# Performance work log

Hardware: AMD Instinct MI355X
Metric: run time of the kernel (lower is better)

## Reference

```python
import jax, jax.numpy as jnp
import numpy as np

HIDDEN = 128
HEADS = 8
HEAD_DIM = HIDDEN // HEADS  # 16
N_NODE_TYPES = 3
N_EDGE_TYPES = 5
N_SRC = 50000
N_DST = 50000
N_EDGES = 800000
SCALE = float(np.sqrt(HEAD_DIM))


def setup_inputs() -> dict:
    key = jax.random.key(0)
    ks = jax.random.split(key, 12)
    lim = 1.0 / np.sqrt(HIDDEN)  # torch Linear default init range
    # xavier_uniform for [H, d, d] relation tensors: gain*sqrt(6/(fan_in+fan_out))
    xav = float(np.sqrt(6.0 / (HEAD_DIM + HEAD_DIM)))
    return {
        "x_src": jax.random.normal(ks[0], (N_SRC, HIDDEN), jnp.float32),
        "x_dst": jax.random.normal(ks[1], (N_DST, HIDDEN), jnp.float32),
        "edge_index": jax.random.randint(ks[2], (2, N_EDGES), 0, N_DST),
        "src_type": 0,
        "edge_type": 1,
        "dst_type": 2,
        "k_w": jax.random.uniform(ks[3], (N_NODE_TYPES, HIDDEN, HIDDEN), jnp.float32, -lim, lim),
        "k_b": jax.random.uniform(ks[4], (N_NODE_TYPES, HIDDEN), jnp.float32, -lim, lim),
        "q_w": jax.random.uniform(ks[5], (N_NODE_TYPES, HIDDEN, HIDDEN), jnp.float32, -lim, lim),
        "q_b": jax.random.uniform(ks[6], (N_NODE_TYPES, HIDDEN), jnp.float32, -lim, lim),
        "v_w": jax.random.uniform(ks[7], (N_NODE_TYPES, HIDDEN, HIDDEN), jnp.float32, -lim, lim),
        "v_b": jax.random.uniform(ks[8], (N_NODE_TYPES, HIDDEN), jnp.float32, -lim, lim),
        "relation_att": jax.random.uniform(ks[9], (N_EDGE_TYPES, HEADS, HEAD_DIM, HEAD_DIM), jnp.float32, -xav, xav),
        "relation_msg": jax.random.uniform(ks[10], (N_EDGE_TYPES, HEADS, HEAD_DIM, HEAD_DIM), jnp.float32, -xav, xav),
        "relation_pri": jnp.ones((N_EDGE_TYPES, HEADS), jnp.float32),
    }


def reference(x_src, x_dst, edge_index, src_type, edge_type, dst_type,
              k_w, k_b, q_w, q_b, v_w, v_b,
              relation_att, relation_msg, relation_pri):
    n_dst = x_dst.shape[0]
    # relation-specific node projections (torch Linear: x @ W.T + b)
    k = (x_src @ k_w[src_type].T + k_b[src_type]).reshape(-1, HEADS, HEAD_DIM)
    v = (x_src @ v_w[src_type].T + v_b[src_type]).reshape(-1, HEADS, HEAD_DIM)
    q = (x_dst @ q_w[dst_type].T + q_b[dst_type]).reshape(-1, HEADS, HEAD_DIM)

    src_idx, dst_idx = edge_index[0], edge_index[1]
    # gather + per-edge relation matmul: [E, H, d]
    k_edge = jnp.einsum('ehi,hio->eho', k[src_idx], relation_att[edge_type])
    att = (k_edge * q[dst_idx]).sum(-1) / SCALE + relation_pri[edge_type][None, :]  # [E, H]

    # segmented softmax over incoming edges per dst node.
    # torch scatter_reduce amax starts from a zero-initialized buffer -> max(0, seg_max)
    seg_max = jnp.maximum(jax.ops.segment_max(att, dst_idx, num_segments=n_dst), 0.0)
    att_exp = jnp.exp(att - seg_max[dst_idx])
    seg_sum = jnp.maximum(jax.ops.segment_sum(att_exp, dst_idx, num_segments=n_dst), 1e-8)
    att_n = att_exp / seg_sum[dst_idx]  # [E, H]

    # messages + weighted scatter-add aggregation
    msg = jnp.einsum('ehi,hio->eho', v[src_idx], relation_msg[edge_type])  # [E, H, d]
    out = jax.ops.segment_sum(att_n[..., None] * msg, dst_idx, num_segments=n_dst)
    return out.reshape(n_dst, HIDDEN)
```

## Files before the change

### kernel.cpp

```cpp
#include <hip/hip_runtime.h>

#define HIDDEN 128
#define HEADS 8
#define HDIM 16
#define BW 64

typedef unsigned int uint;
typedef unsigned short ushort;
typedef __attribute__((ext_vector_type(8))) short bfrag;
typedef __attribute__((ext_vector_type(4))) float f32x4;

__device__ inline ushort f2bf(float f) {
    uint u = __float_as_uint(f);
    uint r = ((u >> 16) & 1u) + 0x7fffu;
    return (ushort)((u + r) >> 16);
}
__device__ inline float bf2f(ushort h) { return __uint_as_float((uint)h << 16); }
__device__ inline float bfl(uint u) { return __uint_as_float(u << 16); }
__device__ inline float bfh(uint u) { return __uint_as_float(u & 0xffff0000u); }

__device__ inline int frag_addr(int k, int n) {
    int ks = k >> 5, kr = k & 31, nt = n >> 4;
    int lane = ((kr >> 3) << 4) | (n & 15);
    return ((ks * 8 + nt) * 64 + lane) * 8 + (kr & 7);
}

__global__ void k1a_weights_zero(
    const float* __restrict__ k_w, const float* __restrict__ k_b,
    const float* __restrict__ q_w, const float* __restrict__ q_b,
    const float* __restrict__ v_w, const float* __restrict__ v_b,
    const float* __restrict__ r_att, const float* __restrict__ r_msg,
    const int* __restrict__ stp, const int* __restrict__ etp, const int* __restrict__ dtp,
    ushort* __restrict__ WkHi, ushort* __restrict__ WvHi, ushort* __restrict__ WqHi,
    float* __restrict__ bk, float* __restrict__ bv, float* __restrict__ bq,
    int* __restrict__ deg, int n_dst)
{
    int idx = blockIdx.x * 256 + threadIdx.x;
    for (int i = idx; i < n_dst; i += 64 * 256) deg[i] = 0;

    int st = stp[0], et = etp[0], dt = dtp[0];
    int c = idx >> 7, j = idx & 127;
    int h = j >> 4, o = j & 15;
    const float* kw = k_w + (size_t)st * HIDDEN * HIDDEN;
    const float* vw = v_w + (size_t)st * HIDDEN * HIDDEN;
    const float* ra = r_att + (size_t)et * HEADS * HDIM * HDIM + h * HDIM * HDIM + o;
    const float* rm = r_msg + (size_t)et * HEADS * HDIM * HDIM + h * HDIM * HDIM + o;
    float sk = 0.f, sv = 0.f;
#pragma unroll
    for (int i = 0; i < HDIM; ++i) {
        sk += kw[(h * HDIM + i) * HIDDEN + c] * ra[i * HDIM];
        sv += vw[(h * HDIM + i) * HIDDEN + c] * rm[i * HDIM];
    }
    float sq = q_w[(size_t)dt * HIDDEN * HIDDEN + (size_t)j * HIDDEN + c];
    int fa = frag_addr(c, j);
    WkHi[fa] = f2bf(sk);
    WvHi[fa] = f2bf(sv);
    WqHi[fa] = f2bf(sq);
    if (idx < HIDDEN) {
        float sb = 0.f, sbv = 0.f;
#pragma unroll
        for (int i = 0; i < HDIM; ++i) {
            sb  += k_b[st * HIDDEN + h * HDIM + i] * ra[i * HDIM];
            sbv += v_b[st * HIDDEN + h * HDIM + i] * rm[i * HDIM];
        }
        bk[idx] = sb;
        bv[idx] = sbv;
        bq[idx] = q_b[dt * HIDDEN + idx];
    }
}

__global__ __launch_bounds__(256, 5) void k1b_proj_countfill(
    const float* __restrict__ x_src, const float* __restrict__ x_dst,
    const ushort* __restrict__ WkHi, const ushort* __restrict__ WvHi,
    const ushort* __restrict__ WqHi,
    const float* __restrict__ bk, const float* __restrict__ bv,
    const float* __restrict__ bq,
    ushort* __restrict__ kr16, ushort* __restrict__ vm16,
    float* __restrict__ qout, int n_src, int n_dst, int nsb, int nprojb,
    const int* __restrict__ ei, int* __restrict__ deg,
    ushort* __restrict__ bucket, int n_edges, int nfb)
{
    __shared__ float xs[32 * 132];
    int blk = blockIdx.x;

    if (blk & 1) {
        int fidx = blk >> 1;
        if (fidx >= nfb) return;
        int e = fidx * 256 + threadIdx.x;
        if (e >= n_edges) return;
        int s = ei[e];
        int d = ei[n_edges + e];
        int r = atomicAdd(&deg[d], 1);
        if (r < BW) bucket[(size_t)d * BW + r] = (ushort)s;
        return;
    }

    int pidx = blk >> 1;
    if (pidx >= nprojb) return;
    int is_src = (pidx < nsb) ? 1 : 0;
    int brow0 = (is_src ? pidx : pidx - nsb) * 32;
    int n = is_src ? n_src : n_dst;
    const float* x = is_src ? x_src : x_dst;
    int t = threadIdx.x;

    {
        const float4* xg = (const float4*)x;
#pragma unroll
        for (int k = 0; k < 4; ++k) {
            int fi = t + k * 256;
            int r = fi >> 5, c4 = fi & 31;
            int row = brow0 + r;
            float4 v = xg[(size_t)(row < n ? row : n - 1) * 32 + c4];
            *(float4*)&xs[r * 132 + c4 * 4] = v;
        }
    }
    __syncthreads();

    int w = t >> 6, l = t & 63;
    int l15 = l & 15, kgrp = l >> 4;
    int nthalf = w & 1;
    int rtile = w >> 1;
    int rowbase = brow0 + rtile * 16;

    bfrag ahi[4];
#pragma unroll
    for (int ks = 0; ks < 4; ++ks) {
        const float* xr = &xs[(rtile * 16 + l15) * 132 + ks * 32 + kgrp * 8];
        float4 x0 = *(const float4*)xr;
        float4 x1 = *(const float4*)(xr + 4);
        float xv[8] = {x0.x, x0.y, x0.z, x0.w, x1.x, x1.y, x1.z, x1.w};
#pragma unroll
        for (int b = 0; b < 8; ++b) {
            ahi[ks][b] = (short)f2bf(xv[b]);
        }
    }

    if (is_src) {
        const bfrag* Fk = (const bfrag*)WkHi;
        const bfrag* Fv = (const bfrag*)WvHi;
#pragma unroll
        for (int nt4 = 0; nt4 < 4; ++nt4) {
            int nt = nthalf * 4 + nt4;
            f32x4 ak = (f32x4){0.f, 0.f, 0.f, 0.f};
            f32x4 av = (f32x4){0.f, 0.f, 0.f, 0.f};
#pragma unroll
            for (int ks = 0; ks < 4; ++ks) {
                int fi = (ks * 8 + nt) * 64 + l;
                bfrag wk = Fk[fi], wv = Fv[fi];
                ak = __builtin_amdgcn_mfma_f32_16x16x32_bf16(ahi[ks], wk, ak, 0, 0, 0);
                av = __builtin_amdgcn_mfma_f32_16x16x32_bf16(ahi[ks], wv, av, 0, 0, 0);
            }
            int col = nt * 16 + l15;
            float bkc = bk[col], bvc = bv[col];
#pragma unroll
            for (int r = 0; r < 4; ++r) {
                int row = rowbase + kgrp * 4 + r;
                if (row < n) {
                    kr16[(size_t)row * HIDDEN + col] = f2bf(ak[r] + bkc);
                    vm16[(size_t)row * HIDDEN + col] = f2bf(av[r] + bvc);
                }
            }
        }
    } else {
        const bfrag* Fq = (const bfrag*)WqHi;
#pragma unroll
        for (int nt4 = 0; nt4 < 4; ++nt4) {
            int nt = nthalf * 4 + nt4;
            f32x4 aq = (f32x4){0.f, 0.f, 0.f, 0.f};
#pragma unroll
            for (int ks = 0; ks < 4; ++ks) {
                int fi = (ks * 8 + nt) * 64 + l;
                bfrag wq = Fq[fi];
                aq = __builtin_amdgcn_mfma_f32_16x16x32_bf16(ahi[ks], wq, aq, 0, 0, 0);
            }
            int col = nt * 16 + l15;
            float bqc = bq[col];
#pragma unroll
            for (int r = 0; r < 4; ++r) {
                int row = rowbase + kgrp * 4 + r;
                if (row < n) qout[(size_t)row * HIDDEN + col] = aq[r] + bqc;
            }
        }
    }
}

__global__ void fused_gather_kernel(const ushort* __restrict__ kr16,
                                    const ushort* __restrict__ vm16,
                                    const float* __restrict__ q,
                                    const float* __restrict__ pri,
                                    const int* __restrict__ etp,
                                    const int* __restrict__ deg,
                                    const ushort* __restrict__ bucket,
                                    float* __restrict__ out, int n_dst)
{
    int wave = (int)((blockIdx.x * 256 + threadIdx.x) >> 6);
    int l = threadIdx.x & 63;
    if (wave >= n_dst) return;
    int d = wave;
    int h = l >> 3;
    int e = l & 7;
    int len = deg[d]; if (len > BW) len = BW;
    const ushort* buck = bucket + (size_t)d * BW;

    const float4* qp = (const float4*)(q + (size_t)d * HIDDEN + h * HDIM);
    float4 q0 = qp[0], q1 = qp[1], q2 = qp[2], q3 = qp[3];
    float prih = pri[etp[0] * HEADS + h];

    float m = 0.0f;
    float ssum = 0.0f;
    float accx = 0.0f, accy = 0.0f;

    for (int i0 = 0; i0 < len; i0 += 16) {
        int ieA = i0 + e, ieB = i0 + 8 + e;
        bool vA = ieA < len, vB = ieB < len;
        bool useB = (i0 + 8) < len;
        int sA = buck[vA ? ieA : 0];
        int sB = buck[vB ? ieB : 0];

        const uint4* kpA = (const uint4*)(kr16 + (size_t)sA * HIDDEN + h * HDIM);
        const uint4* kpB = (const uint4*)(kr16 + (size_t)sB * HIDDEN + h * HDIM);
        uint4 kaA = kpA[0], kbA = kpA[1];
        uint4 kaB = kpB[0], kbB = kpB[1];

        uint vvA[8], vvB[8];
#pragma unroll
        for (int ee = 0; ee < 8; ++ee) {
            int se = __shfl(sA, ee);
            vvA[ee] = *(const uint*)(vm16 + (size_t)se * HIDDEN + 2 * l);
        }
        if (useB) {
#pragma unroll
            for (int ee = 0; ee < 8; ++ee) {
                int se = __shfl(sB, ee);
                vvB[ee] = *(const uint*)(vm16 + (size_t)se * HIDDEN + 2 * l);
            }
        }

        float dotA =
            bfl(kaA.x) * q0.x + bfh(kaA.x) * q0.y + bfl(kaA.y) * q0.z + bfh(kaA.y) * q0.w +
            bfl(kaA.z) * q1.x + bfh(kaA.z) * q1.y + bfl(kaA.w) * q1.z + bfh(kaA.w) * q1.w +
            bfl(kbA.x) * q2.x + bfh(kbA.x) * q2.y + bfl(kbA.y) * q2.z + bfh(kbA.y) * q2.w +
            bfl(kbA.z) * q3.x + bfh(kbA.z) * q3.y + bfl(kbA.w) * q3.z + bfh(kbA.w) * q3.w;
        float dotB =
            bfl(kaB.x) * q0.x + bfh(kaB.x) * q0.y + bfl(kaB.y) * q0.z + bfh(kaB.y) * q0.w +
            bfl(kaB.z) * q1.x + bfh(kaB.z) * q1.y + bfl(kaB.w) * q1.z + bfh(kaB.w) * q1.w +
            bfl(kbB.x) * q2.x + bfh(kbB.x) * q2.y + bfl(kbB.y) * q2.z + bfh(kbB.y) * q2.w +
            bfl(kbB.z) * q3.x + bfh(kbB.z) * q3.y + bfl(kbB.w) * q3.z + bfh(kbB.w) * q3.w;

        float aA = vA ? (dotA * 0.25f + prih) : -3.0e38f;
        float aB = vB ? (dotB * 0.25f + prih) : -3.0e38f;

        float pm = fmaxf(aA, aB);
        pm = fmaxf(pm, __shfl_xor(pm, 1));
        pm = fmaxf(pm, __shfl_xor(pm, 2));
        pm = fmaxf(pm, __shfl_xor(pm, 4));
        float mnew = fmaxf(m, pm);
        float c = __expf(m - mnew);
        float wA = vA ? __expf(aA - mnew) : 0.0f;
        float wB = vB ? __expf(aB - mnew) : 0.0f;
        float S = wA + wB;
        S += __shfl_xor(S, 1);
        S += __shfl_xor(S, 2);
        S += __shfl_xor(S, 4);
        ssum = ssum * c + S;
        accx *= c;
        accy *= c;
        m = mnew;

#pragma unroll
        for (int ee = 0; ee < 8; ++ee) {
            float we = __shfl(wA, (l & 56) | ee);
            accx += we * bfl(vvA[ee]);
            accy += we * bfh(vvA[ee]);
        }
        if (useB) {
#pragma unroll
            for (int ee = 0; ee < 8; ++ee) {
                float we = __shfl(wB, (l & 56) | ee);
                accx += we * bfl(vvB[ee]);
                accy += we * bfh(vvB[ee]);
            }
        }
    }

    float inv = 1.0f / fmaxf(ssum, 1e-8f);
    float2 o; o.x = accx * inv; o.y = accy * inv;
    *(float2*)(out + (size_t)d * HIDDEN + 2 * l) = o;
}

extern "C" void kernel_launch(void* const* d_in, const int* in_sizes, int n_in,
                              void* d_out, int out_size, void* d_ws, size_t ws_size,
                              hipStream_t stream)
{
    const float* x_src = (const float*)d_in[0];
    const float* x_dst = (const float*)d_in[1];
    const int*   ei    = (const int*)d_in[2];
    const int*   stp   = (const int*)d_in[3];
    const int*   etp   = (const int*)d_in[4];
    const int*   dtp   = (const int*)d_in[5];
    const float* k_w   = (const float*)d_in[6];
    const float* k_b   = (const float*)d_in[7];
    const float* q_w   = (const float*)d_in[8];
    const float* q_b   = (const float*)d_in[9];
    const float* v_w   = (const float*)d_in[10];
    const float* v_b   = (const float*)d_in[11];
    const float* r_att = (const float*)d_in[12];
    const float* r_msg = (const float*)d_in[13];
    const float* r_pri = (const float*)d_in[14];

    int n_src   = in_sizes[0] / HIDDEN;
    int n_dst   = in_sizes[1] / HIDDEN;
    int n_edges = in_sizes[2] / 2;
    float* out = (float*)d_out;

    char* p = (char*)d_ws;
    ushort* kr16 = (ushort*)p;            p += (size_t)n_src * HIDDEN * sizeof(ushort);
    ushort* vm16 = (ushort*)p;            p += (size_t)n_src * HIDDEN * sizeof(ushort);
    float*  qv   = (float*)p;             p += (size_t)n_dst * HIDDEN * sizeof(float);
    ushort* bucket = (ushort*)p;          p += (size_t)n_dst * BW * sizeof(ushort);
    int* deg     = (int*)p;               p += (size_t)n_dst * sizeof(int);
    float* bk = (float*)p;                p += HIDDEN * sizeof(float);
    float* bv = (float*)p;                p += HIDDEN * sizeof(float);
    float* bq = (float*)p;                p += HIDDEN * sizeof(float);
    ushort* WkHi = (ushort*)p;            p += HIDDEN * HIDDEN * sizeof(ushort);
    ushort* WvHi = (ushort*)p;            p += HIDDEN * HIDDEN * sizeof(ushort);
    ushort* WqHi = (ushort*)p;            p += HIDDEN * HIDDEN * sizeof(ushort);

    k1a_weights_zero<<<64, 256, 0, stream>>>(
        k_w, k_b, q_w, q_b, v_w, v_b, r_att, r_msg, stp, etp, dtp,
        WkHi, WvHi, WqHi, bk, bv, bq, deg, n_dst);

    int nsb = (n_src + 31) / 32;
    int ndb = (n_dst + 31) / 32;
    int nprojb = nsb + ndb;
    int nfb = (n_edges + 255) / 256;
    int bigger = nprojb > nfb ? nprojb : nfb;
    k1b_proj_countfill<<<2 * bigger, 256, 0, stream>>>(
        x_src, x_dst, WkHi, WvHi, WqHi, bk, bv, bq,
        kr16, vm16, qv, n_src, n_dst, nsb, nprojb,
        ei, deg, bucket, n_edges, nfb);

    fused_gather_kernel<<<(int)(((size_t)n_dst * 64 + 255) / 256), 256, 0, stream>>>(
        kr16, vm16, qv, r_pri, etp, deg, bucket, out, n_dst);
}
```

Baseline: 128.4 us.

## Replace global-atomic bucket fill with two-pass destination binning via shared memory

Measured after the change: 139.4 us. 8.6% more time.

```diff
diff --git a/kernel.cpp b/kernel.cpp
--- a/kernel.cpp
+++ b/kernel.cpp
@@ -4,6 +4,8 @@
 #define HEADS 8
 #define HDIM 16
 #define BW 64
+#define BINSH 8
+#define BINCAP 4608
 
 typedef unsigned int uint;
 typedef unsigned short ushort;
@@ -25,19 +27,16 @@
     return ((ks * 8 + nt) * 64 + lane) * 8 + (kr & 7);
 }
 
-__global__ void k1a_weights_zero(
+__global__ void k1a_weights(
     const float* __restrict__ k_w, const float* __restrict__ k_b,
     const float* __restrict__ q_w, const float* __restrict__ q_b,
     const float* __restrict__ v_w, const float* __restrict__ v_b,
     const float* __restrict__ r_att, const float* __restrict__ r_msg,
     const int* __restrict__ stp, const int* __restrict__ etp, const int* __restrict__ dtp,
     ushort* __restrict__ WkHi, ushort* __restrict__ WvHi, ushort* __restrict__ WqHi,
-    float* __restrict__ bk, float* __restrict__ bv, float* __restrict__ bq,
-    int* __restrict__ deg, int n_dst)
+    float* __restrict__ bk, float* __restrict__ bv, float* __restrict__ bq)
 {
     int idx = blockIdx.x * 256 + threadIdx.x;
-    for (int i = idx; i < n_dst; i += 64 * 256) deg[i] = 0;
-
     int st = stp[0], et = etp[0], dt = dtp[0];
     int c = idx >> 7, j = idx & 127;
     int h = j >> 4, o = j & 15;
@@ -69,7 +68,7 @@
     }
 }
 
-__global__ __launch_bounds__(256, 5) void k1b_proj_countfill(
+__global__ __launch_bounds__(256, 5) void k1b_proj_bin(
     const float* __restrict__ x_src, const float* __restrict__ x_dst,
     const ushort* __restrict__ WkHi, const ushort* __restrict__ WvHi,
     const ushort* __restrict__ WqHi,
@@ -77,31 +76,65 @@
     const float* __restrict__ bq,
     ushort* __restrict__ kr16, ushort* __restrict__ vm16,
     float* __restrict__ qout, int n_src, int n_dst, int nsb, int nprojb,
-    const int* __restrict__ ei, int* __restrict__ deg,
-    ushort* __restrict__ bucket, int n_edges, int nfb)
+    const int* __restrict__ ei, uint* __restrict__ gcnt,
+    uint* __restrict__ gbin, int n_edges, int nfb1)
 {
-    __shared__ float xs[32 * 132];
+    __shared__ uint smem[32 * 132];
     int blk = blockIdx.x;
 
-    if (blk & 1) {
-        int fidx = blk >> 1;
-        if (fidx >= nfb) return;
-        int e = fidx * 256 + threadIdx.x;
-        if (e >= n_edges) return;
-        int s = ei[e];
-        int d = ei[n_edges + e];
-        int r = atomicAdd(&deg[d], 1);
-        if (r < BW) bucket[(size_t)d * BW + r] = (ushort)s;
+    if ((blk & 15) == 15) {
+        int fidx = blk >> 4;
+        if (fidx >= nfb1) return;
+        uint* hist  = smem;
+        uint* gbase = smem + 256;
+        uint* cur   = smem + 512;
+        int t = threadIdx.x;
+        hist[t] = 0;
+        cur[t] = 0;
+        __syncthreads();
+
+        int base = fidx * 4096 + t;
+        int mybin[16];
+        uint mypl[16];
+#pragma unroll
+        for (int k = 0; k < 16; ++k) {
+            int e = base + k * 256;
+            if (e < n_edges) {
+                int s = ei[e];
+                int d = ei[n_edges + e];
+                int b = d >> BINSH;
+                mybin[k] = b;
+                mypl[k] = ((uint)(d & 255) << 16) | (uint)s;
+                atomicAdd(&hist[b], 1u);
+            } else {
+                mybin[k] = -1;
+                mypl[k] = 0;
+            }
+        }
+        __syncthreads();
+        uint hv = hist[t];
+        if (hv) gbase[t] = atomicAdd(&gcnt[t], hv);
+        __syncthreads();
+#pragma unroll
+        for (int k = 0; k < 16; ++k) {
+            if (mybin[k] >= 0) {
+                int b = mybin[k];
+                uint r = atomicAdd(&cur[b], 1u);
+                uint pos = gbase[b] + r;
+                if (pos < BINCAP) gbin[(size_t)b * BINCAP + pos] = mypl[k];
+            }
+        }
         return;
     }
 
-    int pidx = blk >> 1;
+    int pidx = blk - (blk >> 4) - (((blk & 15) == 15) ? 1 : 0);
     if (pidx >= nprojb) return;
     int is_src = (pidx < nsb) ? 1 : 0;
     int brow0 = (is_src ? pidx : pidx - nsb) * 32;
     int n = is_src ? n_src : n_dst;
     const float* x = is_src ? x_src : x_dst;
     int t = threadIdx.x;
+    float* xs = (float*)smem;
 
     {
         const float4* xg = (const float4*)x;
@@ -182,6 +215,45 @@
             }
         }
     }
+}
+
+__global__ __launch_bounds__(256) void k2_binfill(
+    const uint* __restrict__ gbin, const uint* __restrict__ gcnt,
+    ushort* __restrict__ bucket, int* __restrict__ deg, int n_dst)
+{
+    __shared__ ushort lb[256 * BW];
+    __shared__ uint lcnt[256];
+    int b = blockIdx.x;
+    int t = threadIdx.x;
+    lcnt[t] = 0;
+    {
+        uint4 z = {0, 0, 0, 0};
+        uint4* lb4 = (uint4*)lb;
+#pragma unroll
+        for (int i = 0; i < 8; ++i) lb4[t + i * 256] = z;
+    }
+    __syncthreads();
+
+    int cnt = (int)gcnt[b];
+    if (cnt > BINCAP) cnt = BINCAP;
+    const uint* seg = gbin + (size_t)b * BINCAP;
+    for (int i = t; i < cnt; i += 256) {
+        uint pl = seg[i];
+        int dl = (int)(pl >> 16);
+        uint r = atomicAdd(&lcnt[dl], 1u);
+        if (r < BW) lb[dl * BW + r] = (ushort)(pl & 0xFFFFu);
+    }
+    __syncthreads();
+
+    int dbase = b << BINSH;
+    int nvalid = n_dst - dbase;
+    if (nvalid > 256) nvalid = 256;
+    if (nvalid <= 0) return;
+    const uint4* src4 = (const uint4*)lb;
+    uint4* dst4 = (uint4*)(bucket + (size_t)dbase * BW);
+    int tot4 = nvalid * 8;
+    for (int i = t; i < tot4; i += 256) dst4[i] = src4[i];
+    if (t < nvalid) deg[dbase + t] = (int)lcnt[t];
 }
 
 __global__ void fused_gather_kernel(const ushort* __restrict__ kr16,
@@ -214,8 +286,8 @@
         int ieA = i0 + e, ieB = i0 + 8 + e;
         bool vA = ieA < len, vB = ieB < len;
         bool useB = (i0 + 8) < len;
-        int sA = buck[vA ? ieA : 0];
-        int sB = buck[vB ? ieB : 0];
+        int sA = vA ? (int)buck[ieA] : (int)buck[0];
+        int sB = vB ? (int)buck[ieB] : (int)buck[0];
 
         const uint4* kpA = (const uint4*)(kr16 + (size_t)sA * HIDDEN + h * HDIM);
         const uint4* kpB = (const uint4*)(kr16 + (size_t)sB * HIDDEN + h * HDIM);
@@ -312,6 +384,7 @@
     int n_dst   = in_sizes[1] / HIDDEN;
     int n_edges = in_sizes[2] / 2;
     float* out = (float*)d_out;
+    int nbins = (n_dst + 255) >> BINSH;
 
     char* p = (char*)d_ws;
     ushort* kr16 = (ushort*)p;            p += (size_t)n_src * HIDDEN * sizeof(ushort);
@@ -319,6 +392,8 @@
     float*  qv   = (float*)p;             p += (size_t)n_dst * HIDDEN * sizeof(float);
     ushort* bucket = (ushort*)p;          p += (size_t)n_dst * BW * sizeof(ushort);
     int* deg     = (int*)p;               p += (size_t)n_dst * sizeof(int);
+    uint* gcnt   = (uint*)p;              p += 256 * sizeof(uint);
+    uint* gbin   = (uint*)p;              p += (size_t)nbins * BINCAP * sizeof(uint);
     float* bk = (float*)p;                p += HIDDEN * sizeof(float);
     float* bv = (float*)p;                p += HIDDEN * sizeof(float);
     float* bq = (float*)p;                p += HIDDEN * sizeof(float);
@@ -326,19 +401,24 @@
     ushort* WvHi = (ushort*)p;            p += HIDDEN * HIDDEN * sizeof(ushort);
     ushort* WqHi = (ushort*)p;            p += HIDDEN * HIDDEN * sizeof(ushort);
 
-    k1a_weights_zero<<<64, 256, 0, stream>>>(
+    hipMemsetAsync(gcnt, 0, 256 * sizeof(uint), stream);
+
+    k1a_weights<<<64, 256, 0, stream>>>(
         k_w, k_b, q_w, q_b, v_w, v_b, r_att, r_msg, stp, etp, dtp,
-        WkHi, WvHi, WqHi, bk, bv, bq, deg, n_dst);
+        WkHi, WvHi, WqHi, bk, bv, bq);
 
     int nsb = (n_src + 31) / 32;
     int ndb = (n_dst + 31) / 32;
     int nprojb = nsb + ndb;
-    int nfb = (n_edges + 255) / 256;
-    int bigger = nprojb > nfb ? nprojb : nfb;
-    k1b_proj_countfill<<<2 * bigger, 256, 0, stream>>>(
+    int nfb1 = (n_edges + 4095) / 4096;
+    int G = nprojb + nfb1;
+    while (G - (G >> 4) < nprojb || (G >> 4) < nfb1) ++G;
+    k1b_proj_bin<<<G, 256, 0, stream>>>(
         x_src, x_dst, WkHi, WvHi, WqHi, bk, bv, bq,
         kr16, vm16, qv, n_src, n_dst, nsb, nprojb,
-        ei, deg, bucket, n_edges, nfb);
+        ei, gcnt, gbin, n_edges, nfb1);
+
+    k2_binfill<<<nbins, 256, 0, stream>>>(gbin, gcnt, bucket, deg, n_dst);
 
     fused_gather_kernel<<<(int)(((size_t)n_dst * 64 + 255) / 256), 256, 0, stream>>>(
         kr16, vm16, qv, r_pri, etp, deg, bucket, out, n_dst);
```
